# Kernel optimization log

Hardware: AMD Instinct MI355X
Metric: run time of the kernel (lower is better)

Reference implementation:

```python
import jax, jax.numpy as jnp
import numpy as np

B, C, T = 64, 128, 500
N_RES, N_CLASSES = 2048, 10
DECAY_RES, DECAY_CLF = 0.9, 0.9
V_TH_RES, V_TH_CLF = 1.0, 1.0


def setup_inputs() -> dict:
    key = jax.random.key(0)
    k1, k2, k3, k4 = jax.random.split(key, 4)
    x = jax.random.normal(k1, (B, C, T), dtype=jnp.float32)
    # learned / fixed parameters sized per init_kwargs
    W_in = jax.random.normal(k2, (N_RES, C), dtype=jnp.float32) * (1.0 / np.sqrt(C))
    W_res = jax.random.normal(k3, (N_RES, N_RES), dtype=jnp.float32) * (1.0 / np.sqrt(N_RES))
    W_clf = jax.random.normal(k4, (N_CLASSES, N_RES), dtype=jnp.float32) * (1.0 / np.sqrt(N_RES))
    return {"x": x, "W_in": W_in, "W_res": W_res, "W_clf": W_clf}


def reference(x, W_in, W_res, W_clf):
    """x: (B, C, T). Returns (spike_counts (B, n_classes), reservoir_spikes_accum (B, n_reservoir)).
    LIF reservoir + single-voter LIF readout, no STDP updates (use_stdp=False path)."""
    Bb = x.shape[0]
    dtype = x.dtype

    def step(carry, x_t):  # x_t: (B, C)
        v_r, s_prev, v_c = carry
        # reservoir LIF: leak + feedforward input + recurrent spike input
        I = x_t @ W_in.T + s_prev @ W_res.T          # (B, N_RES)
        v_r = DECAY_RES * v_r + I
        s = (v_r >= V_TH_RES).astype(dtype)          # spike
        v_r = v_r * (1.0 - s)                        # reset fired neurons
        # classifier (STDPLayer forward, plasticity disabled)
        v_c = DECAY_CLF * v_c + s @ W_clf.T          # (B, N_CLASSES)
        c = (v_c >= V_TH_CLF).astype(dtype)
        v_c = v_c * (1.0 - c)
        return (v_r, s, v_c), (c, s)

    init = (jnp.zeros((Bb, N_RES), dtype),
            jnp.zeros((Bb, N_RES), dtype),
            jnp.zeros((Bb, N_CLASSES), dtype))
    xs = jnp.moveaxis(x, 2, 0)                       # (T, B, C)
    _, (clf_spikes, res_spikes) = jax.lax.scan(step, init, xs)
    spike_counts = clf_spikes.sum(axis=0)            # (B, N_CLASSES)
    reservoir_spikes_accum = res_spikes.sum(axis=0)  # (B, N_RES)
    return spike_counts, reservoir_spikes_accum
```

## Files before the change

### kernel.cpp

```cpp
#include <hip/hip_runtime.h>
#include <cstdint>
#include <cstddef>

#define B_    64
#define C_    128
#define T_    500
#define NRES  2048
#define NCLS  10

#define NWG   256
#define SL    8
#define NT    1024
#define WROW  520
#define WPIT  (4 * WROW)



#define WS_MASK0   0
#define WS_MASK1   16384
#define WS_FLAG    32768
#define WS_ARR     49152
#define WS_WORDS   13312
#define NFLAG      16
#define CHKWG      (NWG - 1)

typedef float v2f __attribute__((ext_vector_type(2)));

struct SMem {
  float    WtT2[SL][WPIT];
  float    WinT2[SL][C_];
  float    xs2[2][B_][C_ + 1];
  unsigned mask[B_][65];
  double   clfred2[2][NCLS];
};

__global__ void zero_ws_kernel(unsigned* __restrict__ p, int n) {
  int i = blockIdx.x * blockDim.x + threadIdx.x;
  if (i < n) p[i] = 0u;
}

#define ACC2(ACC, WB, M0, M1, JB) do {                                        \
  const unsigned _lo = (unsigned)(((int)((M0) << (31 - (JB)))) >> 31) & (WB); \
  const unsigned _hi = (unsigned)(((int)((M1) << (31 - (JB)))) >> 31) & (WB); \
  v2f _m; _m.x = __uint_as_float(_lo); _m.y = __uint_as_float(_hi);           \
  (ACC) = (ACC) + _m;                                                         \
} while (0)

#define BT_STEP(X, D, MLO) do {                                            \
  const unsigned _y = (unsigned)__shfl_xor((int)(X), (D), 64);             \
  (X) = (b & (D)) ? (((X) & ~(MLO)) | ((_y >> (D)) & (MLO)))               \
                  : (((X) & (MLO)) | ((_y << (D)) & ~(MLO)));              \
} while (0)

#define BT_ALL(X) do {                 \
  BT_STEP(X, 16, 0x0000FFFFu);         \
  BT_STEP(X,  8, 0x00FF00FFu);         \
  BT_STEP(X,  4, 0x0F0F0F0Fu);         \
  BT_STEP(X,  2, 0x33333333u);         \
  BT_STEP(X,  1, 0x55555555u);         \
} while (0)

struct SMemRef;

__device__ __forceinline__ float g1_compute(const float* __restrict__ winrow,
                                            const float* __restrict__ xrow) {
  float g1 = 0.f;
  const float4* __restrict__ winp = (const float4*)winrow;
  #pragma unroll 8
  for (int cq = 0; cq < 32; ++cq) {
    const float4 wv = winp[cq];
    const int c = cq * 4;
    g1 = fmaf(xrow[c + 0], wv.x, g1);
    g1 = fmaf(xrow[c + 1], wv.y, g1);
    g1 = fmaf(xrow[c + 2], wv.z, g1);
    g1 = fmaf(xrow[c + 3], wv.w, g1);
  }
  return g1;
}

__global__ void __launch_bounds__(NT, 4)
reservoir_kernel(const float* __restrict__ x, const float* __restrict__ Win,
                 const float* __restrict__ Wres, const float* __restrict__ Wclf,
                 float* __restrict__ out, unsigned char* __restrict__ ws) {
  __shared__ SMem sm;
  const int w   = blockIdx.x;
  const int tid = threadIdx.x;
  const int b   = tid & 63;
  const int wid = tid >> 6;
  const int il  = wid & 7;
  const int h   = wid >> 3;
  const int blk = b & 3;
  const int g   = b >> 2;
  const int bat0 = h * 32 + g * 2;
  const int bat1 = bat0 + 1;
  const int iu  = __builtin_amdgcn_readfirstlane(w * SL + il);
  const int bat = h * 32 + (b & 31);

  unsigned* gm0  = (unsigned*)(ws + WS_MASK0);
  unsigned* gm1  = (unsigned*)(ws + WS_MASK1);
  unsigned* flgb = (unsigned*)(ws + WS_FLAG);
  unsigned* arr  = (unsigned*)(ws + WS_ARR);
  unsigned* myflag = flgb + (w & (NFLAG - 1)) * 256;

  {
    const int j0 = tid * 16;
    #pragma unroll
    for (int r4 = 0; r4 < 4; ++r4) {
      const int j   = j0 + r4 * 4;
      const int il2 = j >> 11;
      const int pos = j & 2047;
      const int bk  = pos >> 9;
      const int s   = pos & 511;
      const float4 v4 = *(const float4*)(Wres + (size_t)(w * SL + il2) * NRES + pos);
      *(float4*)(&sm.WtT2[il2][bk * WROW + s]) = v4;
    }
  }
  {
    const int il2 = tid >> 7, c = tid & 127;
    sm.WinT2[il2][c] = Win[(size_t)(w * SL + il2) * C_ + c];
  }

  float v = 0.f;
  int   cntr = 0;
  double vc = 0.0;
  int   cntc = 0;

  float xv[8];
  {
    const int p0 = tid * 8;
    #pragma unroll
    for (int r = 0; r < 8; ++r) {
      float z = x[(size_t)(p0 + r) * T_ + 0];
      int p = p0 + r;
      sm.xs2[0][p >> 7][p & 127] = z;
    }
    #pragma unroll
    for (int r = 0; r < 8; ++r) xv[r] = x[(size_t)(p0 + r) * T_ + 1];
  }
  __syncthreads();

  float g1cur = 0.f;
  if (b < 32) g1cur = g1_compute(&sm.WinT2[il][0], &sm.xs2[0][bat][0]);

  for (int t = 0; t < T_; ++t) {
    unsigned* gprev = (t & 1) ? gm0 : gm1;
    unsigned* gcur  = (t & 1) ? gm1 : gm0;

    {
      const int i32 = b & 31, hh = b >> 5;
      #pragma unroll
      for (int kk = 0; kk < 4; ++kk) {
        const int k = (wid << 2) | kk;
        unsigned xw = __hip_atomic_load(gprev + (k * 32 + i32) * 2 + hh,
                                        __ATOMIC_RELAXED, __HIP_MEMORY_SCOPE_AGENT);
        BT_ALL(xw);
        sm.mask[b][k] = xw;
      }
    }
    __syncthreads();

    if (t + 1 < T_) {
      const int p0 = tid * 8;
      #pragma unroll
      for (int r = 0; r < 8; ++r) {
        int p = p0 + r;
        sm.xs2[(t + 1) & 1][p >> 7][p & 127] = xv[r];
      }
      if (t + 2 < T_) {
        #pragma unroll
        for (int r = 0; r < 8; ++r) xv[r] = x[(size_t)(p0 + r) * T_ + (t + 2)];
      }
    }

    v2f acc; acc.x = 0.f; acc.y = 0.f;
    {
      const float*    wbase = &sm.WtT2[il][blk * WROW];
      const unsigned* mr0   = &sm.mask[bat0][blk * 16];
      const unsigned* mr1   = &sm.mask[bat1][blk * 16];
      #pragma unroll 4
      for (int wq = 0; wq < 16; ++wq) {
        const unsigned m0 = mr0[wq];
        const unsigned m1 = mr1[wq];
        const float4* q = (const float4*)(wbase + wq * 32);
        #pragma unroll
        for (int jq = 0; jq < 8; ++jq) {
          const float4 w4 = q[jq];
          const int jb = jq * 4;
          ACC2(acc, __float_as_uint(w4.x), m0, m1, jb + 0);
          ACC2(acc, __float_as_uint(w4.y), m0, m1, jb + 1);
          ACC2(acc, __float_as_uint(w4.z), m0, m1, jb + 2);
          ACC2(acc, __float_as_uint(w4.w), m0, m1, jb + 3);
        }
      }
    }
    const float aP = acc.x, aQ = acc.y;

    const float p1 = __shfl_xor(aP, 1), q1 = __shfl_xor(aQ, 1);
    const float p2 = __shfl_xor(aP, 2), q2 = __shfl_xor(aQ, 2);
    const float p3 = __shfl_xor(aP, 3), q3 = __shfl_xor(aQ, 3);
    const float g2u0 = __fadd_rn(__fadd_rn(__fadd_rn(aP, p1), p2), p3);
    const float g2u1 = __fadd_rn(__fadd_rn(__fadd_rn(aQ, q1), q2), q3);

    {
      const int src = (b >> 1) * 4;
      const float r0 = __shfl(g2u0, src, 64);
      const float r1 = __shfl(g2u1, src, 64);
      const float g2m = (b & 1) ? r1 : r0;
      const float I = __fadd_rn(g1cur, g2m);
      v = __fadd_rn(__fmul_rn(0.9f, v), I);
      bool s = (b < 32) && (v >= 1.0f);
      if (s) { v = 0.f; cntr++; }
      unsigned long long bal = __ballot(s);
      if (b == 0)
        __hip_atomic_store(gcur + iu * 2 + h, (unsigned)bal,
                           __ATOMIC_RELAXED, __HIP_MEMORY_SCOPE_AGENT);
    }
    __syncthreads();

    if (tid == 0)
      __hip_atomic_store(arr + w * 4, (unsigned)(t + 1),
                         __ATOMIC_RELEASE, __HIP_MEMORY_SCOPE_AGENT);


    if (t + 1 < T_) {
      if (b < 32)
        g1cur = g1_compute(&sm.WinT2[il][0], &sm.xs2[(t + 1) & 1][bat][0]);
    }

    if (w == CHKWG && wid == 0) {
      const unsigned tgt = (unsigned)(t + 1);
      for (;;) {
        unsigned a0 = __hip_atomic_load(arr + (b +   0) * 4, __ATOMIC_RELAXED,
                                        __HIP_MEMORY_SCOPE_AGENT);
        unsigned a1 = __hip_atomic_load(arr + (b +  64) * 4, __ATOMIC_RELAXED,
                                        __HIP_MEMORY_SCOPE_AGENT);
        unsigned a2 = __hip_atomic_load(arr + (b + 128) * 4, __ATOMIC_RELAXED,
                                        __HIP_MEMORY_SCOPE_AGENT);
        unsigned a3 = __hip_atomic_load(arr + (b + 192) * 4, __ATOMIC_RELAXED,
                                        __HIP_MEMORY_SCOPE_AGENT);
        bool ok = (a0 >= tgt) & (a1 >= tgt) & (a2 >= tgt) & (a3 >= tgt);
        if (__all(ok)) break;
        __builtin_amdgcn_s_sleep(1);
      }
      if (b < NFLAG)
        __hip_atomic_store(flgb + b * 256, (unsigned)(t + 1),
                           __ATOMIC_RELEASE, __HIP_MEMORY_SCOPE_AGENT);
    }

    if (w < B_) {
      if (wid < NCLS) {
        double pc = 0.0;
        if (t > 0) {
          const float* __restrict__ wc = Wclf + (size_t)wid * NRES + b;
          #pragma unroll 4
          for (int q = 0; q < 32; ++q) {
            const unsigned mw = sm.mask[w][(b >> 5) + 2 * q];
            const float wv = wc[q * 64];
            const unsigned keep =
                (unsigned)(((int)(mw << (31 - (b & 31)))) >> 31);
            pc += (double)__uint_as_float(keep & __float_as_uint(wv));
          }
        }
        #pragma unroll
        for (int off = 1; off < 64; off <<= 1)
          pc += __shfl_xor(pc, off, 64);
        if (b == 0) sm.clfred2[t & 1][wid] = pc;
      }

      if (tid < NCLS && t >= 2) {
        vc = 0.9 * vc + sm.clfred2[(t + 1) & 1][tid];
        if (vc >= 1.0) { vc = 0.0; cntc++; }
      }

      if (tid == 0) {
        while (__hip_atomic_load(myflag, __ATOMIC_RELAXED,
                                 __HIP_MEMORY_SCOPE_AGENT) < (unsigned)(t + 1))
          __builtin_amdgcn_s_sleep(1);
      }
      __syncthreads();
    } else {
      while (__hip_atomic_load(myflag, __ATOMIC_RELAXED,
                               __HIP_MEMORY_SCOPE_AGENT) < (unsigned)(t + 1))
        __builtin_amdgcn_s_sleep(1);
    }
  }

  if (w < B_ && tid < NCLS) {
    vc = 0.9 * vc + sm.clfred2[1][tid];
    if (vc >= 1.0) { vc = 0.0; cntc++; }
  }
  {
    const int i32 = b & 31, hh = b >> 5;
    #pragma unroll
    for (int kk = 0; kk < 4; ++kk) {
      const int k = (wid << 2) | kk;
      unsigned xw = __hip_atomic_load(gm1 + (k * 32 + i32) * 2 + hh,
                                      __ATOMIC_RELAXED, __HIP_MEMORY_SCOPE_AGENT);
      BT_ALL(xw);
      sm.mask[b][k] = xw;
    }
  }
  __syncthreads();
  if (w < B_ && wid < NCLS) {
    double pc = 0.0;
    {
      const float* __restrict__ wc = Wclf + (size_t)wid * NRES + b;
      #pragma unroll 4
      for (int q = 0; q < 32; ++q) {
        const unsigned mw = sm.mask[w][(b >> 5) + 2 * q];
        const float wv = wc[q * 64];
        const unsigned keep =
            (unsigned)(((int)(mw << (31 - (b & 31)))) >> 31);
        pc += (double)__uint_as_float(keep & __float_as_uint(wv));
      }
    }
    #pragma unroll
    for (int off = 1; off < 64; off <<= 1)
      pc += __shfl_xor(pc, off, 64);
    if (b == 0) sm.clfred2[0][wid] = pc;
  }
  __syncthreads();
  if (w < B_ && tid < NCLS) {
    vc = 0.9 * vc + sm.clfred2[0][tid];
    if (vc >= 1.0) cntc++;
    out[w * NCLS + tid] = (float)cntc;
  }
  if (b < 32)
    out[B_ * NCLS + (size_t)bat * NRES + w * SL + il] = (float)cntr;
}

extern "C" void kernel_launch(void* const* d_in, const int* in_sizes, int n_in,
                              void* d_out, int out_size, void* d_ws, size_t ws_size,
                              hipStream_t stream) {
  const float* x    = (const float*)d_in[0];
  const float* Win  = (const float*)d_in[1];
  const float* Wres = (const float*)d_in[2];
  const float* Wclf = (const float*)d_in[3];
  float* out = (float*)d_out;
  unsigned char* ws = (unsigned char*)d_ws;

  hipLaunchKernelGGL(zero_ws_kernel, dim3((WS_WORDS + 255) / 256), dim3(256), 0, stream,
                     (unsigned*)ws, WS_WORDS);
  hipLaunchKernelGGL(reservoir_kernel, dim3(NWG), dim3(NT), 0, stream,
                     x, Win, Wres, Wclf, out, ws);
}
```

Baseline: 13.84 ms.

## Double-buffer spike masks to drop per-step barrier and vectorize x staging

The spike-mask shared buffer becomes double-buffered by timestep parity, which lets the kernel drop the `__syncthreads` that ended each step. Every wave now polls the inter-workgroup flag directly instead of one thread polling and then a block barrier. The x staging buffer goes from double to single, with a padded 132-float row pitch so it can be written and read as float4 in the g1 dot product. The aim is to cut per-step barrier latency on the serial 500-step critical path and to reduce LDS instruction count. The cost is 1024 threads spinning on the same global flag instead of one, which adds atomic polling traffic.

```diff
diff --git a/kernel.cpp b/kernel.cpp
--- a/kernel.cpp
+++ b/kernel.cpp
@@ -13,6 +13,7 @@
 #define NT    1024
 #define WROW  520
 #define WPIT  (4 * WROW)
+#define XSP   132
 
 
 
@@ -29,8 +30,8 @@
 struct SMem {
   float    WtT2[SL][WPIT];
   float    WinT2[SL][C_];
-  float    xs2[2][B_][C_ + 1];
-  unsigned mask[B_][65];
+  float    xs[B_][XSP];
+  unsigned maskb[2][B_][65];
   double   clfred2[2][NCLS];
 };
 
@@ -60,20 +61,19 @@
   BT_STEP(X,  1, 0x55555555u);         \
 } while (0)
 
-struct SMemRef;
-
 __device__ __forceinline__ float g1_compute(const float* __restrict__ winrow,
                                             const float* __restrict__ xrow) {
   float g1 = 0.f;
   const float4* __restrict__ winp = (const float4*)winrow;
+  const float4* __restrict__ xrp  = (const float4*)xrow;
   #pragma unroll 8
   for (int cq = 0; cq < 32; ++cq) {
     const float4 wv = winp[cq];
-    const int c = cq * 4;
-    g1 = fmaf(xrow[c + 0], wv.x, g1);
-    g1 = fmaf(xrow[c + 1], wv.y, g1);
-    g1 = fmaf(xrow[c + 2], wv.z, g1);
-    g1 = fmaf(xrow[c + 3], wv.w, g1);
+    const float4 xq = xrp[cq];
+    g1 = fmaf(xq.x, wv.x, g1);
+    g1 = fmaf(xq.y, wv.y, g1);
+    g1 = fmaf(xq.z, wv.z, g1);
+    g1 = fmaf(xq.w, wv.w, g1);
   }
   return g1;
 }
@@ -128,23 +128,27 @@
   float xv[8];
   {
     const int p0 = tid * 8;
-    #pragma unroll
-    for (int r = 0; r < 8; ++r) {
-      float z = x[(size_t)(p0 + r) * T_ + 0];
-      int p = p0 + r;
-      sm.xs2[0][p >> 7][p & 127] = z;
-    }
+    float tmp[8];
+    #pragma unroll
+    for (int r = 0; r < 8; ++r) tmp[r] = x[(size_t)(p0 + r) * T_ + 0];
+    float4 fa, fb;
+    fa.x = tmp[0]; fa.y = tmp[1]; fa.z = tmp[2]; fa.w = tmp[3];
+    fb.x = tmp[4]; fb.y = tmp[5]; fb.z = tmp[6]; fb.w = tmp[7];
+    const int row = p0 >> 7, col = p0 & 127;
+    *(float4*)(&sm.xs[row][col])     = fa;
+    *(float4*)(&sm.xs[row][col + 4]) = fb;
     #pragma unroll
     for (int r = 0; r < 8; ++r) xv[r] = x[(size_t)(p0 + r) * T_ + 1];
   }
   __syncthreads();
 
   float g1cur = 0.f;
-  if (b < 32) g1cur = g1_compute(&sm.WinT2[il][0], &sm.xs2[0][bat][0]);
+  if (b < 32) g1cur = g1_compute(&sm.WinT2[il][0], &sm.xs[bat][0]);
 
   for (int t = 0; t < T_; ++t) {
     unsigned* gprev = (t & 1) ? gm0 : gm1;
     unsigned* gcur  = (t & 1) ? gm1 : gm0;
+    unsigned (* __restrict__ mk)[65] = sm.maskb[t & 1];
 
     {
       const int i32 = b & 31, hh = b >> 5;
@@ -154,18 +158,19 @@
         unsigned xw = __hip_atomic_load(gprev + (k * 32 + i32) * 2 + hh,
                                         __ATOMIC_RELAXED, __HIP_MEMORY_SCOPE_AGENT);
         BT_ALL(xw);
-        sm.mask[b][k] = xw;
+        mk[b][k] = xw;
       }
     }
     __syncthreads();
 
     if (t + 1 < T_) {
       const int p0 = tid * 8;
-      #pragma unroll
-      for (int r = 0; r < 8; ++r) {
-        int p = p0 + r;
-        sm.xs2[(t + 1) & 1][p >> 7][p & 127] = xv[r];
-      }
+      float4 fa, fb;
+      fa.x = xv[0]; fa.y = xv[1]; fa.z = xv[2]; fa.w = xv[3];
+      fb.x = xv[4]; fb.y = xv[5]; fb.z = xv[6]; fb.w = xv[7];
+      const int row = p0 >> 7, col = p0 & 127;
+      *(float4*)(&sm.xs[row][col])     = fa;
+      *(float4*)(&sm.xs[row][col + 4]) = fb;
       if (t + 2 < T_) {
         #pragma unroll
         for (int r = 0; r < 8; ++r) xv[r] = x[(size_t)(p0 + r) * T_ + (t + 2)];
@@ -175,8 +180,8 @@
     v2f acc; acc.x = 0.f; acc.y = 0.f;
     {
       const float*    wbase = &sm.WtT2[il][blk * WROW];
-      const unsigned* mr0   = &sm.mask[bat0][blk * 16];
-      const unsigned* mr1   = &sm.mask[bat1][blk * 16];
+      const unsigned* mr0   = &mk[bat0][blk * 16];
+      const unsigned* mr1   = &mk[bat1][blk * 16];
       #pragma unroll 4
       for (int wq = 0; wq < 16; ++wq) {
         const unsigned m0 = mr0[wq];
@@ -222,10 +227,8 @@
                          __ATOMIC_RELEASE, __HIP_MEMORY_SCOPE_AGENT);
 
 
-    if (t + 1 < T_) {
-      if (b < 32)
-        g1cur = g1_compute(&sm.WinT2[il][0], &sm.xs2[(t + 1) & 1][bat][0]);
-    }
+    if (t + 1 < T_ && b < 32)
+      g1cur = g1_compute(&sm.WinT2[il][0], &sm.xs[bat][0]);
 
     if (w == CHKWG && wid == 0) {
       const unsigned tgt = (unsigned)(t + 1);
@@ -254,7 +257,7 @@
           const float* __restrict__ wc = Wclf + (size_t)wid * NRES + b;
           #pragma unroll 4
           for (int q = 0; q < 32; ++q) {
-            const unsigned mw = sm.mask[w][(b >> 5) + 2 * q];
+            const unsigned mw = mk[w][(b >> 5) + 2 * q];
             const float wv = wc[q * 64];
             const unsigned keep =
                 (unsigned)(((int)(mw << (31 - (b & 31)))) >> 31);
@@ -266,25 +269,18 @@
           pc += __shfl_xor(pc, off, 64);
         if (b == 0) sm.clfred2[t & 1][wid] = pc;
       }
-
       if (tid < NCLS && t >= 2) {
         vc = 0.9 * vc + sm.clfred2[(t + 1) & 1][tid];
         if (vc >= 1.0) { vc = 0.0; cntc++; }
       }
-
-      if (tid == 0) {
-        while (__hip_atomic_load(myflag, __ATOMIC_RELAXED,
-                                 __HIP_MEMORY_SCOPE_AGENT) < (unsigned)(t + 1))
-          __builtin_amdgcn_s_sleep(1);
-      }
-      __syncthreads();
-    } else {
-      while (__hip_atomic_load(myflag, __ATOMIC_RELAXED,
-                               __HIP_MEMORY_SCOPE_AGENT) < (unsigned)(t + 1))
-        __builtin_amdgcn_s_sleep(1);
-    }
-  }
-
+    }
+
+    while (__hip_atomic_load(myflag, __ATOMIC_RELAXED,
+                             __HIP_MEMORY_SCOPE_AGENT) < (unsigned)(t + 1))
+      __builtin_amdgcn_s_sleep(1);
+  }
+
+  __syncthreads();
   if (w < B_ && tid < NCLS) {
     vc = 0.9 * vc + sm.clfred2[1][tid];
     if (vc >= 1.0) { vc = 0.0; cntc++; }
@@ -297,7 +293,7 @@
       unsigned xw = __hip_atomic_load(gm1 + (k * 32 + i32) * 2 + hh,
                                       __ATOMIC_RELAXED, __HIP_MEMORY_SCOPE_AGENT);
       BT_ALL(xw);
-      sm.mask[b][k] = xw;
+      sm.maskb[0][b][k] = xw;
     }
   }
   __syncthreads();
@@ -307,7 +303,7 @@
       const float* __restrict__ wc = Wclf + (size_t)wid * NRES + b;
       #pragma unroll 4
       for (int q = 0; q < 32; ++q) {
-        const unsigned mw = sm.mask[w][(b >> 5) + 2 * q];
+        const unsigned mw = sm.maskb[0][w][(b >> 5) + 2 * q];
         const float wv = wc[q * 64];
         const unsigned keep =
             (unsigned)(((int)(mw << (31 - (b & 31)))) >> 31);
```

Result: no change. 13.65 ms (-1.4%).
